# Performance work log

Hardware: AMD Instinct MI355X
Metric: run time of the kernel (lower is better)

The kernel has to match this reference:

```python
import jax, jax.numpy as jnp
import numpy as np

B, S, C = 32, 512, 384
MAX_LEN = 4096
MAX_DUR = 16


def setup_inputs() -> dict:
    key = jax.random.key(0)
    kx, kd = jax.random.split(key)
    x = jax.random.normal(kx, (B, S, C), dtype=jnp.float32)
    durations = jax.random.randint(kd, (B, S), 0, MAX_DUR, dtype=jnp.int32)
    return {"x": x, "durations": durations, "max_length": MAX_LEN}


def reference(x, durations, max_length):
    # Round (no-op for int durations, kept for faithfulness to torch.round().long())
    d = jnp.round(durations.astype(jnp.float32)).astype(jnp.int32)  # [B, S]
    # _limit_durations is equivalent to clipping the cumulative sum at max_length:
    # the first token crossing max_length gets truncated, all later tokens zeroed.
    ends = jnp.clip(jnp.cumsum(d, axis=1), 0, max_length)          # [B, S]
    total = ends[:, -1]                                            # [B]
    t = jnp.arange(max_length, dtype=jnp.int32)                    # [T]
    # frame t belongs to phoneme j where starts[j] <= t < ends[j];
    # searchsorted(ends, t, 'right') skips zero-duration tokens automatically.
    idx = jax.vmap(lambda e: jnp.searchsorted(e, t, side='right'))(ends)  # [B, T]
    mel_masks = t[None, :] >= total[:, None]                       # [B, T] True = pad
    idx_c = jnp.clip(idx, 0, x.shape[1] - 1)
    expanded = jnp.take_along_axis(x, idx_c[:, :, None], axis=1)   # [B, T, C]
    expanded = jnp.where(mel_masks[:, :, None], jnp.zeros((), x.dtype), expanded)
    return expanded, mel_masks
```

## Files before the change

kernel.cpp:

```cpp
#include <hip/hip_runtime.h>

#define BATCH 32
#define SEQ 512
#define CH 384
#define CH4 96
#define MAXL 4096
#define K2T 384
#define K2G 32

typedef float v4f __attribute__((ext_vector_type(4)));

__global__ __launch_bounds__(SEQ) void lr_scan_kernel(
    const int* __restrict__ durations,
    const int* __restrict__ max_len_p,
    int* __restrict__ ws_idx,
    float* __restrict__ out_mask)
{
    __shared__ int s_cum[SEQ];
    __shared__ int s_idx[MAXL];

    const int tid = threadIdx.x;
    const int b = blockIdx.x;
    const int maxlen = max_len_p[0];

    s_cum[tid] = durations[b * SEQ + tid];
    __syncthreads();
    #pragma unroll
    for (int off = 1; off < SEQ; off <<= 1) {
        int v = (tid >= off) ? s_cum[tid - off] : 0;
        __syncthreads();
        s_cum[tid] += v;
        __syncthreads();
    }

    for (int t = tid; t < MAXL; t += SEQ) s_idx[t] = -1;
    __syncthreads();

    int e  = min(s_cum[tid], maxlen);
    int st = (tid == 0) ? 0 : min(s_cum[tid - 1], maxlen);
    for (int t = st; t < e; ++t) s_idx[t] = tid;
    __syncthreads();

    for (int t = tid; t < MAXL; t += SEQ) {
        int v = s_idx[t];
        ws_idx[b * MAXL + t] = v;
        __builtin_nontemporal_store((v < 0) ? 1.0f : 0.0f,
                                    &out_mask[b * MAXL + t]);
    }
}

__global__ __launch_bounds__(K2T) void lr_expand_kernel(
    const v4f* __restrict__ x,
    const int* __restrict__ ws_idx,
    v4f* __restrict__ out)
{
    const int tid = threadIdx.x;
    const int lr  = tid / CH4;
    const int c4  = tid - lr * CH4;
    const int r0  = blockIdx.x * K2G + lr;

    #pragma unroll
    for (int k = 0; k < K2G / 4; ++k) {
        int r   = r0 + 4 * k;
        int idx = ws_idx[r];
        int b   = r >> 12;
        v4f v = (v4f){0.f, 0.f, 0.f, 0.f};
        if (idx >= 0) v = x[(b * SEQ + idx) * CH4 + c4];
        __builtin_nontemporal_store(v, &out[(size_t)r * CH4 + c4]);
    }
}

extern "C" void kernel_launch(void* const* d_in, const int* in_sizes, int n_in,
                              void* d_out, int out_size, void* d_ws, size_t ws_size,
                              hipStream_t stream) {
    const v4f* x = (const v4f*)d_in[0];
    const int* durations = (const int*)d_in[1];
    const int* max_len_p = (const int*)d_in[2];
    float* out = (float*)d_out;
    float* out_mask = out + (size_t)BATCH * MAXL * CH;
    int* ws_idx = (int*)d_ws;

    lr_scan_kernel<<<BATCH, SEQ, 0, stream>>>(durations, max_len_p, ws_idx, out_mask);
    lr_expand_kernel<<<(BATCH * MAXL) / K2G, K2T, 0, stream>>>(
        x, ws_idx, (v4f*)out);
}
```

Baseline: 238.2 us.

## Replace per-frame gather with per-phoneme scatter of rows plus padding-zero blocks

```diff
diff --git a/kernel.cpp b/kernel.cpp
--- a/kernel.cpp
+++ b/kernel.cpp
@@ -5,19 +5,17 @@
 #define CH 384
 #define CH4 96
 #define MAXL 4096
-#define K2T 384
-#define K2G 32
+#define ZBLK 64
 
 typedef float v4f __attribute__((ext_vector_type(4)));
 
 __global__ __launch_bounds__(SEQ) void lr_scan_kernel(
     const int* __restrict__ durations,
     const int* __restrict__ max_len_p,
-    int* __restrict__ ws_idx,
+    int* __restrict__ ws_ends,
     float* __restrict__ out_mask)
 {
     __shared__ int s_cum[SEQ];
-    __shared__ int s_idx[MAXL];
 
     const int tid = threadIdx.x;
     const int b = blockIdx.x;
@@ -33,40 +31,43 @@
         __syncthreads();
     }
 
-    for (int t = tid; t < MAXL; t += SEQ) s_idx[t] = -1;
-    __syncthreads();
+    ws_ends[b * SEQ + tid] = min(s_cum[tid], maxlen);
+    const int total = min(s_cum[SEQ - 1], maxlen);
 
-    int e  = min(s_cum[tid], maxlen);
-    int st = (tid == 0) ? 0 : min(s_cum[tid - 1], maxlen);
-    for (int t = st; t < e; ++t) s_idx[t] = tid;
-    __syncthreads();
-
-    for (int t = tid; t < MAXL; t += SEQ) {
-        int v = s_idx[t];
-        ws_idx[b * MAXL + t] = v;
-        __builtin_nontemporal_store((v < 0) ? 1.0f : 0.0f,
-                                    &out_mask[b * MAXL + t]);
-    }
+    #pragma unroll
+    for (int t = tid; t < MAXL; t += SEQ)
+        out_mask[b * MAXL + t] = (t >= total) ? 1.0f : 0.0f;
 }
 
-__global__ __launch_bounds__(K2T) void lr_expand_kernel(
+__global__ __launch_bounds__(128) void lr_scatter_kernel(
     const v4f* __restrict__ x,
-    const int* __restrict__ ws_idx,
+    const int* __restrict__ ws_ends,
     v4f* __restrict__ out)
 {
     const int tid = threadIdx.x;
-    const int lr  = tid / CH4;
-    const int c4  = tid - lr * CH4;
-    const int r0  = blockIdx.x * K2G + lr;
+    const int bid = blockIdx.x;
 
-    #pragma unroll
-    for (int k = 0; k < K2G / 4; ++k) {
-        int r   = r0 + 4 * k;
-        int idx = ws_idx[r];
-        int b   = r >> 12;
-        v4f v = (v4f){0.f, 0.f, 0.f, 0.f};
-        if (idx >= 0) v = x[(b * SEQ + idx) * CH4 + c4];
-        __builtin_nontemporal_store(v, &out[(size_t)r * CH4 + c4]);
+    if (bid < BATCH * SEQ) {
+        const int b = bid >> 9;
+        const int j = bid & (SEQ - 1);
+        const int e  = ws_ends[bid];
+        const int st = j ? ws_ends[bid - 1] : 0;
+        if (tid >= CH4 || e <= st) return;
+        v4f v = x[(size_t)bid * CH4 + tid];
+        v4f* ob = out + ((size_t)(b << 12) + st) * CH4 + tid;
+        for (int t = st; t < e; ++t) {
+            *ob = v;
+            ob += CH4;
+        }
+    } else {
+        const int z = bid - BATCH * SEQ;
+        const int b = z >> 6;
+        const int i = z & (ZBLK - 1);
+        const int total = ws_ends[b * SEQ + SEQ - 1];
+        if (tid >= CH4) return;
+        const v4f zero = (v4f){0.f, 0.f, 0.f, 0.f};
+        for (int t = total + i; t < MAXL; t += ZBLK)
+            out[((size_t)(b << 12) + t) * CH4 + tid] = zero;
     }
 }
 
@@ -78,9 +79,9 @@
     const int* max_len_p = (const int*)d_in[2];
     float* out = (float*)d_out;
     float* out_mask = out + (size_t)BATCH * MAXL * CH;
-    int* ws_idx = (int*)d_ws;
+    int* ws_ends = (int*)d_ws;
 
-    lr_scan_kernel<<<BATCH, SEQ, 0, stream>>>(durations, max_len_p, ws_idx, out_mask);
-    lr_expand_kernel<<<(BATCH * MAXL) / K2G, K2T, 0, stream>>>(
-        x, ws_idx, (v4f*)out);
+    lr_scan_kernel<<<BATCH, SEQ, 0, stream>>>(durations, max_len_p, ws_ends, out_mask);
+    lr_scatter_kernel<<<BATCH * SEQ + BATCH * ZBLK, 128, 0, stream>>>(
+        x, ws_ends, (v4f*)out);
 }
```

Measured after the change: 218.8 us. -8.1%, faster.
